# Optimization experiments

Hardware: AMD Instinct MI355X
Metric: run time of the kernel (lower is better)

Reference implementation:

```python
import jax, jax.numpy as jnp
import numpy as np

REG_MAX = 16
BOX_W = 7.5
OBJ_W = 1.0
TOPK = 10
EPS = 1e-7


def dfl_decode(x, reg_max):
    # x: [B, 4*reg_max, N] -> expected value of per-side distribution -> [B, N, 4] (xyxy)
    B, C, N = x.shape
    x = x.reshape(B, 4, reg_max, N)
    p = jax.nn.softmax(x, axis=2)
    proj = jnp.arange(reg_max, dtype=x.dtype)
    return jnp.einsum('bkrn,r->bnk', p, proj)


def bbox_ciou(b1, b2):
    # b1: [B,N,1,4], b2: [B,1,M,4], xyxy -> [B,N,M]
    x11, y11, x12, y12 = b1[..., 0], b1[..., 1], b1[..., 2], b1[..., 3]
    x21, y21, x22, y22 = b2[..., 0], b2[..., 1], b2[..., 2], b2[..., 3]
    w1, h1 = x12 - x11, y12 - y11
    w2, h2 = x22 - x21, y22 - y21
    iw = jnp.clip(jnp.minimum(x12, x22) - jnp.maximum(x11, x21), 0.0)
    ih = jnp.clip(jnp.minimum(y12, y22) - jnp.maximum(y11, y21), 0.0)
    inter = iw * ih
    union = w1 * h1 + w2 * h2 - inter + EPS
    iou = inter / union
    cw = jnp.maximum(x12, x22) - jnp.minimum(x11, x21)
    ch = jnp.maximum(y12, y22) - jnp.minimum(y11, y21)
    c2 = cw * cw + ch * ch + EPS
    rho2 = ((x21 + x22 - x11 - x12) ** 2 + (y21 + y22 - y11 - y12) ** 2) * 0.25
    v = (4.0 / (np.pi ** 2)) * (jnp.arctan(w2 / (h2 + EPS)) - jnp.arctan(w1 / (h1 + EPS))) ** 2
    alpha = jax.lax.stop_gradient(v / (v - iou + 1.0 + EPS))
    return iou - rho2 / c2 - alpha * v


def setup_inputs() -> dict:
    key = jax.random.key(0)
    k1, k2, k3, k4 = jax.random.split(key, 4)
    B, N, M = 8, 34000, 64
    boxes = jax.random.normal(k1, (B, 4 * REG_MAX, N), dtype=jnp.float32)
    scores = jax.random.normal(k2, (B, N), dtype=jnp.float32)
    # GT boxes: valid xyxy in roughly the same [0, reg_max) range as decoded preds
    xy = jax.random.uniform(k3, (B, M, 2), dtype=jnp.float32) * 11.0
    wh = jax.random.uniform(k4, (B, M, 2), dtype=jnp.float32) * 4.0 + 0.5
    targets = jnp.concatenate([xy, xy + wh], axis=-1)
    return {'boxes': boxes, 'scores': scores, 'targets': targets}


def reference(boxes, scores, targets):
    B, N = scores.shape
    M = targets.shape[1]
    pb = dfl_decode(boxes, REG_MAX)                     # [B,N,4]
    ciou = bbox_ciou(pb[:, :, None, :], targets[:, None, :, :])  # [B,N,M]
    k = min(TOPK, N)
    topv, topi = jax.lax.top_k(jnp.swapaxes(ciou, 1, 2), k)      # [B,M,k] over anchors
    valid = topv > 0.0
    vals = jnp.where(valid, topv, 0.0)

    def per_batch(idx, val, vld):
        flat_i = idx.reshape(-1)
        iou_t = jnp.zeros((N,), val.dtype).at[flat_i].max(val.reshape(-1))
        pos = jnp.zeros((N,), bool).at[flat_i].max(vld.reshape(-1))
        return iou_t, pos

    iou_target, pos = jax.vmap(per_batch)(topi, vals, valid)     # [B,N]
    posf = pos.astype(iou_target.dtype)
    npos = posf.sum(axis=1)
    box_per = jnp.where(npos > 0,
                        ((1.0 - iou_target) * posf).sum(axis=1) / jnp.maximum(npos, 1.0),
                        0.0)
    box_loss = box_per.sum()
    # BCEWithLogits (mean over anchors), summed over batch
    bce = jnp.maximum(scores, 0.0) - scores * iou_target + jnp.log1p(jnp.exp(-jnp.abs(scores)))
    obj_loss = bce.mean(axis=1).sum()
    total = (BOX_W * box_loss + OBJ_W * obj_loss) / B
    return total, box_loss, obj_loss
```

## Files before the change

### kernel.cpp

```cpp
#include <hip/hip_runtime.h>
#include <math.h>

#define BQ 8
#define MQ 64
#define REGMAX 16
#define KTOP 10
#define EPSQ 1e-7f
#define MBUF 1344

__device__ __forceinline__ float frcp(float x) { return __builtin_amdgcn_rcpf(x); }

#define ST_BYTES 256

__global__ __launch_bounds__(256) void decode_topk_kernel(
    const float* __restrict__ boxes, const float* __restrict__ scores,
    const float* __restrict__ targets, unsigned int* __restrict__ iou_bits,
    uint2* __restrict__ cand, float* __restrict__ acc, int N, int bpb) {
  const int tid = threadIdx.x;
  const int b = blockIdx.x / bpb;
  const int blk = blockIdx.x - b * bpb;
  const int a0 = blk * 256;
  const int w = tid >> 6;
  const int l = tid & 63;

  __shared__ float s_ex[4 * 256];
  __shared__ float4 s_sv[256];
  __shared__ float s_at[256];
  __shared__ int s_ix[256];
  __shared__ float s_hv[4 * MQ * KTOP];
  __shared__ int s_hi[4 * MQ * KTOP];
  __shared__ int s_cnt;
  __shared__ float s_bce;
  if (tid == 0) { s_cnt = 0; s_bce = 0.f; }

  const int na = a0 + l * 4;
  if (na + 3 < N) {
    float4 X[REGMAX];
    const size_t rowbase = ((size_t)b * 4 * REGMAX + w * REGMAX) * (size_t)N + na;
#pragma unroll
    for (int r = 0; r < REGMAX; ++r)
      X[r] = *(const float4*)&boxes[rowbase + (size_t)r * N];
    const float* xf = (const float*)X;
    float ev[4];
#pragma unroll
    for (int a = 0; a < 4; ++a) {
      float mx = xf[a];
#pragma unroll
      for (int r = 1; r < REGMAX; ++r) mx = fmaxf(mx, xf[r * 4 + a]);
      float s = 0.f, ws = 0.f;
#pragma unroll
      for (int r = 0; r < REGMAX; ++r) {
        float e = __expf(xf[r * 4 + a] - mx);
        s += e;
        ws += (float)r * e;
      }
      ev[a] = ws * frcp(s);
    }
    *(float4*)&s_ex[w * 256 + l * 4] = make_float4(ev[0], ev[1], ev[2], ev[3]);
  }
  __syncthreads();

  const int n = a0 + tid;
  float bce0 = 0.f;
  if (n < N) {
    const size_t i = (size_t)b * N + n;
    iou_bits[i] = 0u;
    float sc = scores[i];
    bce0 = fmaxf(sc, 0.f) + log1pf(__expf(-fabsf(sc)));
    float x1 = s_ex[tid], y1 = s_ex[256 + tid];
    float x2 = s_ex[512 + tid], y2 = s_ex[768 + tid];
    float w1 = x2 - x1, h1 = y2 - y1;
    if (w1 > 0.f && h1 > 0.f) {
      int slot = atomicAdd(&s_cnt, 1);
      s_sv[slot] = make_float4(x1, y1, x2, y2);
      s_at[slot] = atanf(w1 * frcp(h1 + EPSQ));
      s_ix[slot] = n;
    }
  }
#pragma unroll
  for (int d = 1; d < 64; d <<= 1) bce0 += __shfl_xor(bce0, d, 64);
  if (l == 0) atomicAdd(&s_bce, bce0);
  __syncthreads();
  const int nsurv = s_cnt;
  if (tid == 0) atomicAdd(&acc[b * 4 + 2], s_bce);

  const float4 t = ((const float4*)targets)[b * MQ + l];
  const float x21 = t.x, y21 = t.y, x22 = t.z, y22 = t.w;
  const float w2 = x22 - x21, h2 = y22 - y21;
  const float atan_t = atanf(w2 * frcp(h2 + EPSQ));
  const float area2 = w2 * h2, sumx2 = x21 + x22, sumy2 = y21 + y22;
  const float CPI = 4.0f / (float)(M_PI * M_PI);

  float hv0 = 0.f, hv1 = 0.f, hv2 = 0.f, hv3 = 0.f, hv4 = 0.f;
  float hv5 = 0.f, hv6 = 0.f, hv7 = 0.f, hv8 = 0.f, hv9 = 0.f;
  int hi0 = 0, hi1 = 0, hi2 = 0, hi3 = 0, hi4 = 0;
  int hi5 = 0, hi6 = 0, hi7 = 0, hi8 = 0, hi9 = 0;

  const int qlen = (nsurv + 3) >> 2;
  const int j0 = w * qlen;
  const int j1 = min(nsurv, j0 + qlen);
  for (int j = j0; j < j1; ++j) {
    float4 p = s_sv[j];
    float pa = s_at[j];
    int ixj = s_ix[j];
    float x11 = p.x, y11 = p.y, x12 = p.z, y12 = p.w;
    float w1 = x12 - x11, h1 = y12 - y11;
    float iw = fmaxf(fminf(x12, x22) - fmaxf(x11, x21), 0.f);
    float ih = fmaxf(fminf(y12, y22) - fmaxf(y11, y21), 0.f);
    float inter = iw * ih;
    float uni = w1 * h1 + area2 - inter + EPSQ;
    float iou = inter * frcp(uni);
    float cw = fmaxf(x12, x22) - fminf(x11, x21);
    float ch = fmaxf(y12, y22) - fminf(y11, y21);
    float c2 = cw * cw + ch * ch + EPSQ;
    float dx = sumx2 - x11 - x12;
    float dy = sumy2 - y11 - y12;
    float rho2 = (dx * dx + dy * dy) * 0.25f;
    float da = atan_t - pa;
    float v = CPI * da * da;
    float alpha = v * frcp(v - iou + 1.f + EPSQ);
    float ciou = iou - rho2 * frcp(c2) - alpha * v;
    if (ciou > hv9) {
      float cv = ciou;
      int ci = ixj;
#define INS(vk, ik)                         \
  {                                         \
    bool gt = cv > vk;                      \
    float tv_ = vk; int ti_ = ik;           \
    vk = gt ? cv : vk; ik = gt ? ci : ik;   \
    cv = gt ? tv_ : cv; ci = gt ? ti_ : ci; \
  }
      INS(hv0, hi0) INS(hv1, hi1) INS(hv2, hi2) INS(hv3, hi3) INS(hv4, hi4)
      INS(hv5, hi5) INS(hv6, hi6) INS(hv7, hi7) INS(hv8, hi8) INS(hv9, hi9)
#undef INS
    }
  }
  const int hb = (w * MQ + l) * KTOP;
  s_hv[hb + 0] = hv0; s_hi[hb + 0] = hi0;
  s_hv[hb + 1] = hv1; s_hi[hb + 1] = hi1;
  s_hv[hb + 2] = hv2; s_hi[hb + 2] = hi2;
  s_hv[hb + 3] = hv3; s_hi[hb + 3] = hi3;
  s_hv[hb + 4] = hv4; s_hi[hb + 4] = hi4;
  s_hv[hb + 5] = hv5; s_hi[hb + 5] = hi5;
  s_hv[hb + 6] = hv6; s_hi[hb + 6] = hi6;
  s_hv[hb + 7] = hv7; s_hi[hb + 7] = hi7;
  s_hv[hb + 8] = hv8; s_hi[hb + 8] = hi8;
  s_hv[hb + 9] = hv9; s_hi[hb + 9] = hi9;
  __syncthreads();

  if (w == 0) {
    const int m = l;
    int p0 = 0, p1 = 0, p2 = 0, p3 = 0;
    const size_t obase = (((size_t)(b * MQ + m)) * bpb + blk) * KTOP;
    for (int r = 0; r < KTOP; ++r) {
      float c0 = s_hv[(0 * MQ + m) * KTOP + p0];
      float c1 = s_hv[(1 * MQ + m) * KTOP + p1];
      float c2m = s_hv[(2 * MQ + m) * KTOP + p2];
      float c3 = s_hv[(3 * MQ + m) * KTOP + p3];
      float best = c0; int bw = 0;
      if (c1 > best) { best = c1; bw = 1; }
      if (c2m > best) { best = c2m; bw = 2; }
      if (c3 > best) { best = c3; bw = 3; }
      int psel = (bw == 0) ? p0 : (bw == 1) ? p1 : (bw == 2) ? p2 : p3;
      int bidx = s_hi[(bw * MQ + m) * KTOP + psel];
      cand[obase + r] = make_uint2(__float_as_uint(best), (unsigned)bidx);
      if (bw == 0) p0 = min(p0 + 1, KTOP - 1);
      else if (bw == 1) p1 = min(p1 + 1, KTOP - 1);
      else if (bw == 2) p2 = min(p2 + 1, KTOP - 1);
      else p3 = min(p3 + 1, KTOP - 1);
    }
  }
}

__device__ __forceinline__ void select_top10(
    float* s_bv, int* s_bi, float* s_winv, int* s_wini,
    int* s_cnt, int c, int tid) {
  if (tid < 64) {
    for (int r = 0; r < KTOP; ++r) {
      float bv = 0.f;
      int bs = 0xffff;
      for (int sl = tid; sl < c; sl += 64) {
        float v = s_bv[sl];
        if (v > bv) { bv = v; bs = sl; }
      }
      unsigned long long key =
          ((unsigned long long)__float_as_uint(bv) << 32) | (unsigned int)bs;
#pragma unroll
      for (int d = 1; d < 64; d <<= 1) {
        unsigned long long o = __shfl_xor(key, d, 64);
        if (o > key) key = o;
      }
      if (tid == 0) {
        float wv = __uint_as_float((unsigned int)(key >> 32));
        int ws = (int)(key & 0xffffu);
        s_winv[r] = wv;
        if (wv > 0.f && ws != 0xffff) {
          s_wini[r] = s_bi[ws];
          s_bv[ws] = 0.f;
        } else {
          s_wini[r] = 0;
        }
      }
    }
    if (tid < KTOP) { s_bv[tid] = s_winv[tid]; s_bi[tid] = s_wini[tid]; }
    if (tid == 0) *s_cnt = KTOP;
  }
}

__global__ __launch_bounds__(256) void merge_kernel(
    const uint2* __restrict__ cand, const float* __restrict__ scores,
    unsigned int* __restrict__ iou_bits, float* __restrict__ acc,
    int N, int bpb) {
  const int bm = blockIdx.x;
  const int b = bm >> 6;
  const int tid = threadIdx.x;
  const int NC = bpb * KTOP;

  __shared__ float s_bv[MBUF];
  __shared__ int s_bi[MBUF];
  __shared__ float s_winv[KTOP];
  __shared__ int s_wini[KTOP];
  __shared__ int s_cnt;
  if (tid == 0) s_cnt = 0;
  __syncthreads();

  const uint2* base = cand + (size_t)bm * NC;
  for (int k = tid; k < NC; k += 256) {
    uint2 e = base[k];
    float v = __uint_as_float(e.x);
    if (v > 0.f) {
      int slot = atomicAdd(&s_cnt, 1);
      if (slot < MBUF) { s_bv[slot] = v; s_bi[slot] = (int)e.y; }
    }
  }
  __syncthreads();
  int c = min(s_cnt, MBUF);
  __syncthreads();
  if (c > KTOP) {
    select_top10(s_bv, s_bi, s_winv, s_wini, &s_cnt, c, tid);
    __syncthreads();
    c = KTOP;
  }
  if (tid < KTOP && tid < c) {
    float v = s_bv[tid];
    if (v > 0.f) {
      int ix = s_bi[tid];
      unsigned int vb = __float_as_uint(v);
      unsigned int old = atomicMax(&iou_bits[(size_t)b * N + ix], vb);
      if (old < vb) {
        float vold = __uint_as_float(old);
        bool was = (old != 0u);
        atomicAdd(&acc[b * 4 + 0], was ? (vold - v) : (1.f - v));
        if (!was) atomicAdd(&acc[b * 4 + 1], 1.f);
        atomicAdd(&acc[b * 4 + 2], -scores[(size_t)b * N + ix] * (v - vold));
      }
    }
  }
}

__global__ void finalize_kernel(const float* __restrict__ acc,
                                float* __restrict__ out, int N) {
  if (threadIdx.x == 0 && blockIdx.x == 0) {
    float box = 0.f, obj = 0.f;
    for (int bb = 0; bb < BQ; ++bb) {
      float sb = acc[bb * 4 + 0];
      float np = acc[bb * 4 + 1];
      float sc = acc[bb * 4 + 2];
      box += (np > 0.f) ? sb / fmaxf(np, 1.f) : 0.f;
      obj += sc / (float)N;
    }
    out[0] = (7.5f * box + obj) / (float)BQ;
    out[1] = box;
    out[2] = obj;
  }
}

extern "C" void kernel_launch(void* const* d_in, const int* in_sizes, int n_in,
                              void* d_out, int out_size, void* d_ws, size_t ws_size,
                              hipStream_t stream) {
  const float* boxes = (const float*)d_in[0];
  const float* scores = (const float*)d_in[1];
  const float* targets = (const float*)d_in[2];
  float* out = (float*)d_out;
  const int N = in_sizes[1] / BQ;

  const int bpb = (N + 255) / 256;

  char* ws = (char*)d_ws;
  size_t cand_bytes = (size_t)BQ * MQ * bpb * KTOP * sizeof(uint2);
  size_t iou_bytes = (size_t)BQ * N * sizeof(unsigned int);

  uint2* cand = (uint2*)ws;                    ws += cand_bytes;
  unsigned int* iou_bits = (unsigned int*)ws;  ws += iou_bytes;
  float* state = (float*)ws;

  hipMemsetAsync(state, 0, ST_BYTES, stream);

  decode_topk_kernel<<<BQ * bpb, 256, 0, stream>>>(boxes, scores, targets,
                                                   iou_bits, cand, state, N, bpb);
  merge_kernel<<<BQ * MQ, 256, 0, stream>>>(cand, scores, iou_bits, state, N, bpb);
  finalize_kernel<<<1, 64, 0, stream>>>(state, out, N);
}
```

Before: 139.5 us.

## Stage DFL logits via LDS and write candidates in contiguous block-major layout

The decode phase now loads the box logits through an LDS staging buffer, so each thread decodes one anchor's four sides from shared memory instead of holding 64 registers' worth of float4 loads. Shared buffers are aliased into two regions to cut LDS footprint. Per-block top-k candidates are gathered in LDS and written out as one contiguous chunk per block instead of scattered per-target strided stores. The merge kernel reads with the new block-major layout and drops the MBUF clamp, which risks overflowing the shared buffer if more candidates than MBUF survive.

Measured after the change: 143.1 us. 1.03x slower.

```diff
diff --git a/kernel.cpp b/kernel.cpp
--- a/kernel.cpp
+++ b/kernel.cpp
@@ -23,42 +23,50 @@
   const int w = tid >> 6;
   const int l = tid & 63;
 
-  __shared__ float s_ex[4 * 256];
-  __shared__ float4 s_sv[256];
-  __shared__ float s_at[256];
-  __shared__ int s_ix[256];
-  __shared__ float s_hv[4 * MQ * KTOP];
-  __shared__ int s_hi[4 * MQ * KTOP];
+  __shared__ float s_r1[5120];
+  __shared__ float s_r2[1664];
   __shared__ int s_cnt;
   __shared__ float s_bce;
+  float* stage = s_r1;
+  float* s_hv = s_r1;
+  int* s_hi = (int*)(s_r1 + 2560);
+  float4* s_sv = (float4*)s_r2;
+  float* s_at = s_r2 + 1024;
+  int* s_ix = (int*)(s_r2 + 1280);
+  uint2* s_mg = (uint2*)s_r2;
+
   if (tid == 0) { s_cnt = 0; s_bce = 0.f; }
 
-  const int na = a0 + l * 4;
-  if (na + 3 < N) {
-    float4 X[REGMAX];
-    const size_t rowbase = ((size_t)b * 4 * REGMAX + w * REGMAX) * (size_t)N + na;
-#pragma unroll
-    for (int r = 0; r < REGMAX; ++r)
-      X[r] = *(const float4*)&boxes[rowbase + (size_t)r * N];
-    const float* xf = (const float*)X;
-    float ev[4];
-#pragma unroll
-    for (int a = 0; a < 4; ++a) {
-      float mx = xf[a];
-#pragma unroll
-      for (int r = 1; r < REGMAX; ++r) mx = fmaxf(mx, xf[r * 4 + a]);
-      float s = 0.f, ws = 0.f;
-#pragma unroll
-      for (int r = 0; r < REGMAX; ++r) {
-        float e = __expf(xf[r * 4 + a] - mx);
-        s += e;
-        ws += (float)r * e;
-      }
-      ev[a] = ws * frcp(s);
-    }
-    *(float4*)&s_ex[w * 256 + l * 4] = make_float4(ev[0], ev[1], ev[2], ev[3]);
-  }
-  __syncthreads();
+  float out[4];
+  const int c4 = a0 + l * 4;
+  const bool cok = (c4 < N);
+#pragma unroll
+  for (int k = 0; k < 4; ++k) {
+#pragma unroll
+    for (int i = 0; i < 4; ++i) {
+      const int r = w + i * 4;
+      float4 v = make_float4(0.f, 0.f, 0.f, 0.f);
+      if (cok)
+        v = *(const float4*)&boxes[(size_t)(b * 64 + k * 16 + r) * (size_t)N + c4];
+      *(float4*)&stage[r * 256 + l * 4] = v;
+    }
+    __syncthreads();
+    float x[REGMAX];
+#pragma unroll
+    for (int r = 0; r < REGMAX; ++r) x[r] = stage[r * 256 + tid];
+    float mx = x[0];
+#pragma unroll
+    for (int r = 1; r < REGMAX; ++r) mx = fmaxf(mx, x[r]);
+    float s = 0.f, ws = 0.f;
+#pragma unroll
+    for (int r = 0; r < REGMAX; ++r) {
+      float e = __expf(x[r] - mx);
+      s += e;
+      ws += (float)r * e;
+    }
+    out[k] = ws * frcp(s);
+    __syncthreads();
+  }
 
   const int n = a0 + tid;
   float bce0 = 0.f;
@@ -67,8 +75,7 @@
     iou_bits[i] = 0u;
     float sc = scores[i];
     bce0 = fmaxf(sc, 0.f) + log1pf(__expf(-fabsf(sc)));
-    float x1 = s_ex[tid], y1 = s_ex[256 + tid];
-    float x2 = s_ex[512 + tid], y2 = s_ex[768 + tid];
+    float x1 = out[0], y1 = out[1], x2 = out[2], y2 = out[3];
     float w1 = x2 - x1, h1 = y2 - y1;
     if (w1 > 0.f && h1 > 0.f) {
       int slot = atomicAdd(&s_cnt, 1);
@@ -151,7 +158,6 @@
   if (w == 0) {
     const int m = l;
     int p0 = 0, p1 = 0, p2 = 0, p3 = 0;
-    const size_t obase = (((size_t)(b * MQ + m)) * bpb + blk) * KTOP;
     for (int r = 0; r < KTOP; ++r) {
       float c0 = s_hv[(0 * MQ + m) * KTOP + p0];
       float c1 = s_hv[(1 * MQ + m) * KTOP + p1];
@@ -163,13 +169,16 @@
       if (c3 > best) { best = c3; bw = 3; }
       int psel = (bw == 0) ? p0 : (bw == 1) ? p1 : (bw == 2) ? p2 : p3;
       int bidx = s_hi[(bw * MQ + m) * KTOP + psel];
-      cand[obase + r] = make_uint2(__float_as_uint(best), (unsigned)bidx);
+      s_mg[m * KTOP + r] = make_uint2(__float_as_uint(best), (unsigned)bidx);
       if (bw == 0) p0 = min(p0 + 1, KTOP - 1);
       else if (bw == 1) p1 = min(p1 + 1, KTOP - 1);
       else if (bw == 2) p2 = min(p2 + 1, KTOP - 1);
       else p3 = min(p3 + 1, KTOP - 1);
     }
   }
+  __syncthreads();
+  uint2* obase = cand + (size_t)(b * bpb + blk) * (MQ * KTOP);
+  for (int sl = tid; sl < MQ * KTOP; sl += 256) obase[sl] = s_mg[sl];
 }
 
 __device__ __forceinline__ void select_top10(
@@ -213,6 +222,7 @@
     int N, int bpb) {
   const int bm = blockIdx.x;
   const int b = bm >> 6;
+  const int m = bm & 63;
   const int tid = threadIdx.x;
   const int NC = bpb * KTOP;
 
@@ -224,17 +234,19 @@
   if (tid == 0) s_cnt = 0;
   __syncthreads();
 
-  const uint2* base = cand + (size_t)bm * NC;
-  for (int k = tid; k < NC; k += 256) {
-    uint2 e = base[k];
+  for (int k2 = tid; k2 < NC; k2 += 256) {
+    int blkk = k2 / KTOP;
+    int r = k2 - blkk * KTOP;
+    uint2 e = cand[((size_t)(b * bpb + blkk) * MQ + m) * KTOP + r];
     float v = __uint_as_float(e.x);
     if (v > 0.f) {
       int slot = atomicAdd(&s_cnt, 1);
-      if (slot < MBUF) { s_bv[slot] = v; s_bi[slot] = (int)e.y; }
-    }
-  }
-  __syncthreads();
-  int c = min(s_cnt, MBUF);
+      s_bv[slot] = v;
+      s_bi[slot] = (int)e.y;
+    }
+  }
+  __syncthreads();
+  int c = s_cnt;
   __syncthreads();
   if (c > KTOP) {
     select_top10(s_bv, s_bi, s_winv, s_wini, &s_cnt, c, tid);
@@ -287,7 +299,7 @@
   const int bpb = (N + 255) / 256;
 
   char* ws = (char*)d_ws;
-  size_t cand_bytes = (size_t)BQ * MQ * bpb * KTOP * sizeof(uint2);
+  size_t cand_bytes = (size_t)BQ * bpb * MQ * KTOP * sizeof(uint2);
   size_t iou_bytes = (size_t)BQ * N * sizeof(unsigned int);
 
   uint2* cand = (uint2*)ws;                    ws += cand_bytes;
```
